# Kernel tuning notes

Measured on AMD Instinct MI355X. Metric: run time of the kernel, lower is better.

## Reference

```python
import jax, jax.numpy as jnp
import numpy as np

WEIGHT = 0.1
THRESH = 0.3
MARGIN = 0.1


def setup_inputs() -> dict:
    key = jax.random.key(0)
    k1, k2 = jax.random.split(key)
    B = 8388608
    predictions = jax.random.uniform(k1, (B, 4), dtype=jnp.float32)
    relative_times = jax.random.uniform(k2, (B, 1), dtype=jnp.float32)
    return {"predictions": predictions, "relative_times": relative_times}


def reference(predictions, relative_times):
    # predictions: (B, 4) -> columns [Non-POI, POI4, POI5, POI6]
    p4 = predictions[:, 1]
    p5 = predictions[:, 2]
    p6 = predictions[:, 3]
    t = relative_times[:, 0]

    m45 = (p4 > THRESH) & (p5 > THRESH)
    m56 = (p5 > THRESH) & (p6 > THRESH)
    m456 = m45 & (p6 > THRESH)

    term45 = jax.nn.relu(MARGIN - (p5 * t - p4 * t))
    term56 = jax.nn.relu(MARGIN - (p6 * t - p5 * t))
    dist_4_5 = jnp.abs(p5 - p4)
    dist_5_6 = jnp.abs(p6 - p5)
    term_order = jax.nn.relu(dist_4_5 - dist_5_6 + MARGIN)

    total = (jnp.sum(jnp.where(m45, term45, 0.0))
             + jnp.sum(jnp.where(m56, term56, 0.0))
             + jnp.sum(jnp.where(m456, term_order, 0.0)))
    count = (jnp.sum(m45) + jnp.sum(m56) + jnp.sum(m456)).astype(predictions.dtype)

    loss = jnp.where(count > 0, total / jnp.maximum(count, 1.0), total)
    return WEIGHT * loss
```

## Files before the change

### kernel.cpp

```cpp
#include <hip/hip_runtime.h>

#define WEIGHT 0.1f
#define THRESH 0.3f
#define MARGIN 0.1f

#define NBLOCKS 2048
#define NTHREADS 256


__device__ __forceinline__ void row_terms(float4 p, float t,
                                          float& acc, unsigned int& cnt) {
    bool g4 = p.y > THRESH;
    bool g5 = p.z > THRESH;
    bool g6 = p.w > THRESH;
    bool m45  = g4 && g5;
    bool m56  = g5 && g6;
    bool m456 = m45 && g6;

    float term45 = fmaxf(MARGIN - (p.z * t - p.y * t), 0.0f);
    float term56 = fmaxf(MARGIN - (p.w * t - p.z * t), 0.0f);
    float d45 = fabsf(p.z - p.y);
    float d56 = fabsf(p.w - p.z);
    float torder = fmaxf(d45 - d56 + MARGIN, 0.0f);

    acc += (m45  ? term45 : 0.0f)
         + (m56  ? term56 : 0.0f)
         + (m456 ? torder : 0.0f);
    cnt += (unsigned)m45 + (unsigned)m56 + (unsigned)m456;
}

__global__ __launch_bounds__(NTHREADS) void tc_main_kernel(
        const float4* __restrict__ pred,
        const float*  __restrict__ times,
        double*       __restrict__ blk_tot,
        unsigned int* __restrict__ blk_cnt,
        int n) {
    float local = 0.0f;
    unsigned int cnt = 0;

    const int stride = gridDim.x * blockDim.x;
    int i = blockIdx.x * blockDim.x + threadIdx.x;

    for (; i + 3 * stride < n; i += 4 * stride) {
        float4 p0 = pred[i];
        float4 p1 = pred[i + stride];
        float4 p2 = pred[i + 2 * stride];
        float4 p3 = pred[i + 3 * stride];
        float t0 = times[i];
        float t1 = times[i + stride];
        float t2 = times[i + 2 * stride];
        float t3 = times[i + 3 * stride];
        row_terms(p0, t0, local, cnt);
        row_terms(p1, t1, local, cnt);
        row_terms(p2, t2, local, cnt);
        row_terms(p3, t3, local, cnt);
    }
    for (; i < n; i += stride) {
        row_terms(pred[i], times[i], local, cnt);
    }

    double dl = (double)local;
    for (int o = 32; o > 0; o >>= 1) {
        dl  += __shfl_down(dl, o, 64);
        cnt += __shfl_down(cnt, o, 64);
    }

    __shared__ double       s_tot[NTHREADS / 64];
    __shared__ unsigned int s_cnt[NTHREADS / 64];
    int wave = threadIdx.x >> 6;
    int lane = threadIdx.x & 63;
    if (lane == 0) { s_tot[wave] = dl; s_cnt[wave] = cnt; }
    __syncthreads();

    if (threadIdx.x == 0) {
        double bt = 0.0;
        unsigned int bc = 0;
        for (int w = 0; w < NTHREADS / 64; ++w) { bt += s_tot[w]; bc += s_cnt[w]; }
        blk_tot[blockIdx.x] = bt;
        blk_cnt[blockIdx.x] = bc;
    }
}

__global__ __launch_bounds__(NTHREADS) void tc_finalize_kernel(
        const double*       __restrict__ blk_tot,
        const unsigned int* __restrict__ blk_cnt,
        float* __restrict__ out) {
    double dl = 0.0;
    unsigned long long cl = 0;
    for (int i = threadIdx.x; i < NBLOCKS; i += NTHREADS) {
        dl += blk_tot[i];
        cl += blk_cnt[i];
    }
    for (int o = 32; o > 0; o >>= 1) {
        dl += __shfl_down(dl, o, 64);
        cl += __shfl_down(cl, o, 64);
    }
    __shared__ double             s_tot[NTHREADS / 64];
    __shared__ unsigned long long s_cnt[NTHREADS / 64];
    int wave = threadIdx.x >> 6;
    int lane = threadIdx.x & 63;
    if (lane == 0) { s_tot[wave] = dl; s_cnt[wave] = cl; }
    __syncthreads();
    if (threadIdx.x == 0) {
        double total = 0.0;
        unsigned long long count = 0;
        for (int w = 0; w < NTHREADS / 64; ++w) { total += s_tot[w]; count += s_cnt[w]; }
        double c = (double)count;
        double loss = (c > 0.0) ? (total / fmax(c, 1.0)) : total;
        out[0] = (float)((double)WEIGHT * loss);
    }
}

extern "C" void kernel_launch(void* const* d_in, const int* in_sizes, int n_in,
                              void* d_out, int out_size, void* d_ws, size_t ws_size,
                              hipStream_t stream) {
    const float4* pred  = (const float4*)d_in[0];
    const float*  times = (const float*)d_in[1];
    int n = in_sizes[1];

    double*       blk_tot = (double*)d_ws;
    unsigned int* blk_cnt = (unsigned int*)((char*)d_ws + NBLOCKS * sizeof(double));

    tc_main_kernel<<<NBLOCKS, NTHREADS, 0, stream>>>(pred, times, blk_tot, blk_cnt, n);
    tc_finalize_kernel<<<1, NTHREADS, 0, stream>>>(blk_tot, blk_cnt, (float*)d_out);
}
```

Baseline: 215.5 us.

## Assign contiguous row chunks per thread with vectorized time loads

Replaces the grid-stride loop with a fixed layout where each thread processes 8 consecutive rows, loading them as independent float4 reads and reading the times column as two float4 vectors. The grid size is now derived from n, and finalize takes the block count as a parameter. This aims to raise memory-level parallelism and cut scalar time loads, at the cost of strided per-instruction access and more partial sums to reduce.

```diff
diff --git a/kernel.cpp b/kernel.cpp
--- a/kernel.cpp
+++ b/kernel.cpp
@@ -4,8 +4,8 @@
 #define THRESH 0.3f
 #define MARGIN 0.1f
 
-#define NBLOCKS 2048
 #define NTHREADS 256
+#define ROWS_PER_THREAD 8
 
 
 __device__ __forceinline__ void row_terms(float4 p, float t,
@@ -31,32 +31,31 @@
 
 __global__ __launch_bounds__(NTHREADS) void tc_main_kernel(
         const float4* __restrict__ pred,
-        const float*  __restrict__ times,
+        const float4* __restrict__ times4,
         double*       __restrict__ blk_tot,
         unsigned int* __restrict__ blk_cnt,
         int n) {
     float local = 0.0f;
     unsigned int cnt = 0;
 
-    const int stride = gridDim.x * blockDim.x;
-    int i = blockIdx.x * blockDim.x + threadIdx.x;
+    const long base = ((long)blockIdx.x * NTHREADS + threadIdx.x) * ROWS_PER_THREAD;
 
-    for (; i + 3 * stride < n; i += 4 * stride) {
-        float4 p0 = pred[i];
-        float4 p1 = pred[i + stride];
-        float4 p2 = pred[i + 2 * stride];
-        float4 p3 = pred[i + 3 * stride];
-        float t0 = times[i];
-        float t1 = times[i + stride];
-        float t2 = times[i + 2 * stride];
-        float t3 = times[i + 3 * stride];
-        row_terms(p0, t0, local, cnt);
-        row_terms(p1, t1, local, cnt);
-        row_terms(p2, t2, local, cnt);
-        row_terms(p3, t3, local, cnt);
-    }
-    for (; i < n; i += stride) {
-        row_terms(pred[i], times[i], local, cnt);
+    if (base + ROWS_PER_THREAD <= n) {
+        float4 p[ROWS_PER_THREAD];
+#pragma unroll
+        for (int r = 0; r < ROWS_PER_THREAD; ++r) p[r] = pred[base + r];
+        float4 t0 = times4[(base >> 2) + 0];
+        float4 t1 = times4[(base >> 2) + 1];
+
+        float tt[ROWS_PER_THREAD] = { t0.x, t0.y, t0.z, t0.w,
+                                      t1.x, t1.y, t1.z, t1.w };
+#pragma unroll
+        for (int r = 0; r < ROWS_PER_THREAD; ++r)
+            row_terms(p[r], tt[r], local, cnt);
+    } else {
+        const float* times = (const float*)times4;
+        for (long i = base; i < n; ++i)
+            row_terms(pred[i], times[i], local, cnt);
     }
 
     double dl = (double)local;
@@ -84,10 +83,11 @@
 __global__ __launch_bounds__(NTHREADS) void tc_finalize_kernel(
         const double*       __restrict__ blk_tot,
         const unsigned int* __restrict__ blk_cnt,
-        float* __restrict__ out) {
+        float* __restrict__ out,
+        int nblocks) {
     double dl = 0.0;
     unsigned long long cl = 0;
-    for (int i = threadIdx.x; i < NBLOCKS; i += NTHREADS) {
+    for (int i = threadIdx.x; i < nblocks; i += NTHREADS) {
         dl += blk_tot[i];
         cl += blk_cnt[i];
     }
@@ -114,13 +114,16 @@
 extern "C" void kernel_launch(void* const* d_in, const int* in_sizes, int n_in,
                               void* d_out, int out_size, void* d_ws, size_t ws_size,
                               hipStream_t stream) {
-    const float4* pred  = (const float4*)d_in[0];
-    const float*  times = (const float*)d_in[1];
+    const float4* pred   = (const float4*)d_in[0];
+    const float4* times4 = (const float4*)d_in[1];
     int n = in_sizes[1];
 
+    int rows_per_block = NTHREADS * ROWS_PER_THREAD;
+    int nblocks = (n + rows_per_block - 1) / rows_per_block;
+
     double*       blk_tot = (double*)d_ws;
-    unsigned int* blk_cnt = (unsigned int*)((char*)d_ws + NBLOCKS * sizeof(double));
+    unsigned int* blk_cnt = (unsigned int*)((char*)d_ws + (size_t)nblocks * sizeof(double));
 
-    tc_main_kernel<<<NBLOCKS, NTHREADS, 0, stream>>>(pred, times, blk_tot, blk_cnt, n);
-    tc_finalize_kernel<<<1, NTHREADS, 0, stream>>>(blk_tot, blk_cnt, (float*)d_out);
+    tc_main_kernel<<<nblocks, NTHREADS, 0, stream>>>(pred, times4, blk_tot, blk_cnt, n);
+    tc_finalize_kernel<<<1, NTHREADS, 0, stream>>>(blk_tot, blk_cnt, (float*)d_out, nblocks);
 }
```

New measurement: 223.1 us. 3.6% more time.
